# Performance work log

Hardware: AMD Instinct MI355X
Metric: run time of the kernel (lower is better)

Reference implementation:

```python
import jax, jax.numpy as jnp
import numpy as np

M, N, D = 512, 4096, 128
H = N // D  # 32
L = 4096   # cache length


def setup_inputs() -> dict:
    key = jax.random.key(0)
    ks = jax.random.split(key, 6)
    s = 1.0 / np.sqrt(N)
    return {
        "X": jax.random.normal(ks[0], (M, N), jnp.float32),
        "W_q": jax.random.normal(ks[1], (N, N), jnp.float32) * s,
        "W_k": jax.random.normal(ks[2], (N, N), jnp.float32) * s,
        "W_v": jax.random.normal(ks[3], (N, N), jnp.float32) * s,
        "cache_K": jax.random.normal(ks[4], (H, L, D), jnp.float32),
        "cache_V": jax.random.normal(ks[5], (H, L, D), jnp.float32),
        "P": 3584,
    }


def reference(X, W_q, W_k, W_v, cache_K, cache_V, P):
    # nn.Linear(N, N, bias=False): y = x @ W.T
    q = (X @ W_q.T).reshape(M, H, D).transpose(1, 0, 2)  # [H, M, D]
    k = (X @ W_k.T).reshape(M, H, D).transpose(1, 0, 2)  # [H, M, D]
    v = (X @ W_v.T).reshape(M, H, D).transpose(1, 0, 2)  # [H, M, D]
    # KV-cache write at position P (static slice under jit for fixed P)
    cK = jax.lax.dynamic_update_slice(cache_K, k, (0, P, 0))  # [H, L, D]
    cV = jax.lax.dynamic_update_slice(cache_V, v, (0, P, 0))
    # attention over the full cache, no 1/sqrt(D) scaling (faithful to source)
    scores = jnp.einsum("hmd,hld->hml", q, cK)   # [H, M, L]
    weights = jax.nn.softmax(scores, axis=-1)
    out = jnp.einsum("hml,hld->hmd", weights, cV)  # [H, M, D]
    return out.transpose(1, 0, 2).reshape(M, H * D)  # [M, N]
```

## Files before the change

kernel.cpp:

```cpp
#include <hip/hip_runtime.h>
#include <hip/hip_fp16.h>

typedef _Float16 f16x8 __attribute__((ext_vector_type(8)));
typedef float    f32x4 __attribute__((ext_vector_type(4)));

#define MFMA16(a,b,c) __builtin_amdgcn_mfma_f32_16x16x32_f16(a,b,c,0,0,0)

__device__ __forceinline__ void gload_lds16(const void* g, void* l) {
  __builtin_amdgcn_global_load_lds(
      (const __attribute__((address_space(1))) void*)g,
      (__attribute__((address_space(3))) void*)l, 16, 0, 0);
}

__global__ void cvt_f32_f16(const float* __restrict__ src,
                            _Float16* __restrict__ dst, int n8) {
  int i = blockIdx.x * blockDim.x + threadIdx.x;
  int stride = gridDim.x * blockDim.x;
  for (; i < n8; i += stride) {
    const float4* s = (const float4*)src + 2 * (size_t)i;
    float4 a = s[0], b = s[1];
    f16x8 o;
    o[0]=(_Float16)a.x; o[1]=(_Float16)a.y; o[2]=(_Float16)a.z; o[3]=(_Float16)a.w;
    o[4]=(_Float16)b.x; o[5]=(_Float16)b.y; o[6]=(_Float16)b.z; o[7]=(_Float16)b.w;
    ((f16x8*)dst)[i] = o;
  }
}

__global__ __launch_bounds__(256) void cvt_transpose_v(const float* __restrict__ src,
                                                       _Float16* __restrict__ dst) {
  __shared__ _Float16 t[64][72];
  const int b = blockIdx.x;
  const int h = b >> 7, rest = b & 127;
  const int lt = rest >> 1, dt = rest & 1;
  const int l0 = lt * 64, d0 = dt * 64;
  const int tid = threadIdx.x;
  const int r = tid >> 4, c4 = (tid & 15) * 4;
#pragma unroll
  for (int i = 0; i < 4; i++) {
    int l = r + i * 16;
    float4 v = *(const float4*)&src[((size_t)h * 4096 + l0 + l) * 128 + d0 + c4];
    t[c4 + 0][l] = (_Float16)v.x;
    t[c4 + 1][l] = (_Float16)v.y;
    t[c4 + 2][l] = (_Float16)v.z;
    t[c4 + 3][l] = (_Float16)v.w;
  }
  __syncthreads();
  const int d = tid >> 2, lc = (tid & 3) * 16;
#pragma unroll
  for (int i = 0; i < 2; i++) {
    f16x8 o = *(const f16x8*)&t[d][lc + i * 8];
    *(f16x8*)&dst[((size_t)h * 128 + d0 + d) * 4096 + l0 + lc + i * 8] = o;
  }
}

__global__ __launch_bounds__(256) void qkv_gemm(
    const _Float16* __restrict__ X,
    const float* __restrict__ Wq,
    const float* __restrict__ Wk,
    const float* __restrict__ Wv,
    _Float16* __restrict__ Q16,
    _Float16* __restrict__ Kc,
    _Float16* __restrict__ Vt16,
    const int* __restrict__ Pp)
{
  __shared__ __align__(16) _Float16 As[128 * 64];
  __shared__ __align__(16) _Float16 Bs[64 * 64];
  const int bid = blockIdx.x;
  const int xcd = bid & 7, s = bid >> 3;
  const int nt = xcd * 24 + (s >> 2);
  const int mt = s & 3;
  const int m0 = mt * 128, n0 = nt * 64;
  const int tid = threadIdx.x, wave = tid >> 6, lane = tid & 63;
  const int g = lane >> 4, c = lane & 15;
  const int wr = wave >> 1, wc = wave & 1;
  const float* Wp = (n0 < 4096) ? Wq : ((n0 < 8192) ? Wk : Wv);
  const int n0l = n0 & 4095;
  const int ar  = lane >> 3;
  const int acs = (lane & 7) * 16;
  const int brow = tid >> 2;
  const int bc32 = (tid & 3) * 16;
  const float* wsrc = Wp + (size_t)(n0l + brow) * 4096 + bc32;
  const int bsw = (brow & 7) << 4;
  float4 breg[4];
#pragma unroll
  for (int i = 0; i < 4; i++) breg[i] = *(const float4*)(wsrc + i * 4);

  f32x4 acc[4][2] = {};
  for (int k0 = 0; k0 < 4096; k0 += 64) {
    __syncthreads();
#pragma unroll
    for (int p = 0; p < 4; p++) {
      int chunk = wave * 4 + p;
      int row = chunk * 8 + ar;
      gload_lds16((const char*)(X + (size_t)(m0 + row) * 4096 + k0) + (acs ^ ((row & 7) << 4)),
                  (char*)As + chunk * 1024);
    }
    {
      const float* bv = (const float*)breg;
      f16x8 h0, h1;
#pragma unroll
      for (int i = 0; i < 8; i++) { h0[i] = (_Float16)bv[i]; h1[i] = (_Float16)bv[8 + i]; }
      char* rb = (char*)Bs + brow * 128;
      *(f16x8*)(rb + (((tid & 3) * 32)      ^ bsw)) = h0;
      *(f16x8*)(rb + (((tid & 3) * 32 + 16) ^ bsw)) = h1;
      if (k0 + 64 < 4096) {
        const float* ns = wsrc + k0 + 64;
#pragma unroll
        for (int i = 0; i < 4; i++) breg[i] = *(const float4*)(ns + i * 4);
      }
    }
    __syncthreads();
    f16x8 af[2][4], bf[2][2];
#pragma unroll
    for (int mi = 0; mi < 4; mi++) {
      int row = wr * 64 + mi * 16 + c;
      int sw = (row & 7) << 4;
#pragma unroll
      for (int kc = 0; kc < 2; kc++)
        af[kc][mi] = *(const f16x8*)((const char*)As + row * 128 + ((kc * 64 + g * 16) ^ sw));
    }
#pragma unroll
    for (int ni = 0; ni < 2; ni++) {
      int row = wc * 32 + ni * 16 + c;
      int sw = (row & 7) << 4;
#pragma unroll
      for (int kc = 0; kc < 2; kc++)
        bf[kc][ni] = *(const f16x8*)((const char*)Bs + row * 128 + ((kc * 64 + g * 16) ^ sw));
    }
#pragma unroll
    for (int kc = 0; kc < 2; kc++)
#pragma unroll
      for (int mi = 0; mi < 4; mi++)
#pragma unroll
        for (int ni = 0; ni < 2; ni++)
          acc[mi][ni] = MFMA16(af[kc][mi], bf[kc][ni], acc[mi][ni]);
  }
  const int p = Pp[0];
  const int wsel = n0 >> 12;
  const int h = (n0 & 4095) >> 7;
  const int dbase = n0 & 127;
#pragma unroll
  for (int mi = 0; mi < 4; mi++) {
#pragma unroll
    for (int ni = 0; ni < 2; ni++) {
#pragma unroll
      for (int j = 0; j < 4; j++) {
        int m = m0 + wr * 64 + mi * 16 + 4 * g + j;
        int d = dbase + wc * 32 + ni * 16 + c;
        _Float16 hv = (_Float16)acc[mi][ni][j];
        if (wsel == 0)      Q16[(size_t)(h * 512 + m) * 128 + d] = hv;
        else if (wsel == 1) Kc[(size_t)(h * 4096 + p + m) * 128 + d] = hv;
        else                Vt16[((size_t)h * 128 + d) * 4096 + p + m] = hv;
      }
    }
  }
}

__global__ __launch_bounds__(512, 2) void attn_part(
    const _Float16* __restrict__ Q16,
    const _Float16* __restrict__ Kc,
    const _Float16* __restrict__ Vt,
    float* __restrict__ Opart,
    float* __restrict__ Mpart,
    float* __restrict__ Lpart)
{
  __shared__ __align__(16) _Float16 Ks[64 * 128];
  __shared__ __align__(16) _Float16 Vs[128 * 64];
  __shared__ __align__(16) _Float16 Pl[8][32][68];
  const int bid = blockIdx.x;
  const int xcd = bid & 7, s = bid >> 3;
  const int group = xcd * 16 + (s >> 1);
  const int mt = s & 1;
  const int ls = group >> 5, h = group & 31;
  const int m0 = mt * 256;
  const int tid = threadIdx.x, wave = tid >> 6, lane = tid & 63;
  const int g = lane >> 4, c = lane & 15;
  const int mw = m0 + wave * 32;
  const _Float16* Kh  = Kc + (size_t)h * 4096 * 128;
  const _Float16* Vth = Vt + (size_t)h * 128 * 4096;
  f16x8 qf[2][4];
#pragma unroll
  for (int mi = 0; mi < 2; mi++)
#pragma unroll
    for (int kc = 0; kc < 4; kc++)
      qf[mi][kc] = *(const f16x8*)&Q16[(size_t)(h * 512 + mw + mi * 16 + c) * 128 + kc * 32 + g * 8];
  f32x4 o[2][8] = {};
  float mrow[2][4], lrow[2][4];
#pragma unroll
  for (int mi = 0; mi < 2; mi++)
#pragma unroll
    for (int j = 0; j < 4; j++) { mrow[mi][j] = -3e38f; lrow[mi][j] = 0.f; }
  const int klr = lane >> 4, klb = (lane & 15) * 16;
  const int vlr = lane >> 3, vlb = (lane & 7) * 16;

  const int l_begin = ls * 1024;
  for (int l0 = l_begin; l0 < l_begin + 1024; l0 += 64) {
    __syncthreads();
#pragma unroll
    for (int p = 0; p < 2; p++) {
      int chunk = p * 8 + wave;
      int kr = chunk * 4 + klr;
      gload_lds16((const char*)Kh + (size_t)(l0 + kr) * 256 + (klb ^ ((kr & 7) << 4)),
                  (char*)Ks + chunk * 1024);
      int vd = chunk * 8 + vlr;
      gload_lds16((const char*)Vth + (size_t)vd * 8192 + (size_t)l0 * 2 + (vlb ^ ((vd & 7) << 4)),
                  (char*)Vs + chunk * 1024);
    }
    __syncthreads();
    f32x4 sc[2][4] = {};
#pragma unroll
    for (int ni = 0; ni < 4; ni++) {
      int kr = ni * 16 + c;
      f16x8 kf[4];
#pragma unroll
      for (int kc = 0; kc < 4; kc++)
        kf[kc] = *(const f16x8*)((const char*)Ks + kr * 256 + ((kc * 64 + g * 16) ^ ((kr & 7) << 4)));
#pragma unroll
      for (int mi = 0; mi < 2; mi++)
#pragma unroll
        for (int kc = 0; kc < 4; kc++)
          sc[mi][ni] = MFMA16(qf[mi][kc], kf[kc], sc[mi][ni]);
    }
#pragma unroll
    for (int mi = 0; mi < 2; mi++) {
      float scale[4];
#pragma unroll
      for (int j = 0; j < 4; j++) {
        float tm = sc[mi][0][j];
#pragma unroll
        for (int ni = 1; ni < 4; ni++) tm = fmaxf(tm, sc[mi][ni][j]);
        tm = fmaxf(tm, __shfl_xor(tm, 1, 64));
        tm = fmaxf(tm, __shfl_xor(tm, 2, 64));
        tm = fmaxf(tm, __shfl_xor(tm, 4, 64));
        tm = fmaxf(tm, __shfl_xor(tm, 8, 64));
        float mn = fmaxf(mrow[mi][j], tm);
        scale[j] = __expf(mrow[mi][j] - mn);
        mrow[mi][j] = mn;
      }
      float rs[4] = {0.f, 0.f, 0.f, 0.f};
#pragma unroll
      for (int ni = 0; ni < 4; ni++) {
#pragma unroll
        for (int j = 0; j < 4; j++) {
          float pv = __expf(sc[mi][ni][j] - mrow[mi][j]);
          sc[mi][ni][j] = pv;
          rs[j] += pv;
        }
      }
#pragma unroll
      for (int j = 0; j < 4; j++) {
        rs[j] += __shfl_xor(rs[j], 1, 64);
        rs[j] += __shfl_xor(rs[j], 2, 64);
        rs[j] += __shfl_xor(rs[j], 4, 64);
        rs[j] += __shfl_xor(rs[j], 8, 64);
        lrow[mi][j] = lrow[mi][j] * scale[j] + rs[j];
      }
#pragma unroll
      for (int dn = 0; dn < 8; dn++)
#pragma unroll
        for (int j = 0; j < 4; j++) o[mi][dn][j] *= scale[j];
#pragma unroll
      for (int ni = 0; ni < 4; ni++)
#pragma unroll
        for (int j = 0; j < 4; j++)
          Pl[wave][mi * 16 + 4 * g + j][ni * 16 + c] = (_Float16)sc[mi][ni][j];
    }
    f16x8 pa[2][2];
#pragma unroll
    for (int mi = 0; mi < 2; mi++)
#pragma unroll
      for (int kc = 0; kc < 2; kc++)
        pa[mi][kc] = *(const f16x8*)&Pl[wave][mi * 16 + c][kc * 32 + g * 8];
#pragma unroll
    for (int dn = 0; dn < 8; dn++) {
      int vr = dn * 16 + c;
#pragma unroll
      for (int kc = 0; kc < 2; kc++) {
        f16x8 vb = *(const f16x8*)((const char*)Vs + vr * 128 + ((kc * 64 + g * 16) ^ ((vr & 7) << 4)));
#pragma unroll
        for (int mi = 0; mi < 2; mi++)
          o[mi][dn] = MFMA16(pa[mi][kc], vb, o[mi][dn]);
      }
    }
  }
  const size_t pbase = ((size_t)(ls * 32 + h) * 512);
#pragma unroll
  for (int mi = 0; mi < 2; mi++) {
#pragma unroll
    for (int dn = 0; dn < 8; dn++) {
#pragma unroll
      for (int j = 0; j < 4; j++) {
        int m = mw + mi * 16 + 4 * g + j;
        Opart[(pbase + m) * 128 + dn * 16 + c] = o[mi][dn][j];
      }
    }
  }
  if (c == 0) {
#pragma unroll
    for (int mi = 0; mi < 2; mi++)
#pragma unroll
      for (int j = 0; j < 4; j++) {
        int m = mw + mi * 16 + 4 * g + j;
        Mpart[pbase + m] = mrow[mi][j];
        Lpart[pbase + m] = lrow[mi][j];
      }
  }
}

__global__ __launch_bounds__(256) void attn_combine(
    const float* __restrict__ Opart,
    const float* __restrict__ Mpart,
    const float* __restrict__ Lpart,
    float* __restrict__ out)
{
  int idx = blockIdx.x * 256 + threadIdx.x;
  int row = idx >> 5;
  int d4  = idx & 31;
  int h = row >> 9, m = row & 511;
  float Ms[4];
  float mx = -3e38f;
#pragma unroll
  for (int s = 0; s < 4; s++) {
    Ms[s] = Mpart[(size_t)(s * 32 + h) * 512 + m];
    mx = fmaxf(mx, Ms[s]);
  }
  float lsum = 0.f;
  float4 acc = make_float4(0.f, 0.f, 0.f, 0.f);
#pragma unroll
  for (int s = 0; s < 4; s++) {
    float w = __expf(Ms[s] - mx);
    lsum += w * Lpart[(size_t)(s * 32 + h) * 512 + m];
    float4 ov = ((const float4*)(Opart + ((size_t)(s * 32 + h) * 512 + m) * 128))[d4];
    acc.x += w * ov.x; acc.y += w * ov.y; acc.z += w * ov.z; acc.w += w * ov.w;
  }
  float inv = 1.f / lsum;
  float4 r = make_float4(acc.x * inv, acc.y * inv, acc.z * inv, acc.w * inv);
  *(float4*)&out[(size_t)m * 4096 + h * 128 + d4 * 4] = r;
}

extern "C" void kernel_launch(void* const* d_in, const int* in_sizes, int n_in,
                              void* d_out, int out_size, void* d_ws, size_t ws_size,
                              hipStream_t stream) {
  const float* X  = (const float*)d_in[0];
  const float* Wq = (const float*)d_in[1];
  const float* Wk = (const float*)d_in[2];
  const float* Wv = (const float*)d_in[3];
  const float* cK = (const float*)d_in[4];
  const float* cV = (const float*)d_in[5];
  const int*   Pp = (const int*)d_in[6];
  float* out = (float*)d_out;

  char* ws = (char*)d_ws;
  _Float16* X16  = (_Float16*)(ws);
  _Float16* Q16  = (_Float16*)(ws + ((size_t)100 << 20));
  _Float16* K16  = (_Float16*)(ws + ((size_t)104 << 20));
  _Float16* V16t = (_Float16*)(ws + ((size_t)136 << 20));
  float* Opart = (float*)(ws + ((size_t)4  << 20));
  float* Mpart = (float*)(ws + ((size_t)36 << 20));
  float* Lpart = (float*)(ws + ((size_t)37 << 20));

  const int NTH = 256;
  auto cvtl = [&](const float* s, _Float16* d, size_t n) {
    int n8 = (int)(n / 8);
    int grid = (n8 + NTH - 1) / NTH;
    if (grid > 2048) grid = 2048;
    cvt_f32_f16<<<dim3(grid), dim3(NTH), 0, stream>>>(s, d, n8);
  };
  cvtl(X,  X16, (size_t)512 * 4096);
  cvtl(cK, K16, (size_t)32 * 4096 * 128);
  cvt_transpose_v<<<dim3(4096), dim3(NTH), 0, stream>>>(cV, V16t);

  qkv_gemm<<<dim3(768), dim3(256), 0, stream>>>(X16, Wq, Wk, Wv, Q16, K16, V16t, Pp);
  attn_part<<<dim3(256), dim3(512), 0, stream>>>(Q16, K16, V16t, Opart, Mpart, Lpart);
  attn_combine<<<dim3(2048), dim3(256), 0, stream>>>(Opart, Mpart, Lpart, out);
}
```

Measured before the change: 233.0 us.

## Double-buffer LDS in QKV GEMM with one barrier per k-step

Doubles the A and B shared-memory tiles in the QKV projection GEMM so the next k-tile's async global-to-LDS loads and W conversion overlap the MFMA work on the current tile. The two __syncthreads per iteration become a single barrier guarded by hand-written s_waitcnt counters, and s_setprio is raised around the MFMA block. This removes the load-to-compute stall, at the cost of twice the LDS (which may cap occupancy, hinted by launch_bounds 256,3). Correctness depends on the manual vmcnt accounting, and the wrapped last-iteration prefetches do redundant loads.

```diff
diff --git a/kernel.cpp b/kernel.cpp
--- a/kernel.cpp
+++ b/kernel.cpp
@@ -53,7 +53,7 @@
   }
 }
 
-__global__ __launch_bounds__(256) void qkv_gemm(
+__global__ __launch_bounds__(256, 3) void qkv_gemm(
     const _Float16* __restrict__ X,
     const float* __restrict__ Wq,
     const float* __restrict__ Wk,
@@ -63,8 +63,8 @@
     _Float16* __restrict__ Vt16,
     const int* __restrict__ Pp)
 {
-  __shared__ __align__(16) _Float16 As[128 * 64];
-  __shared__ __align__(16) _Float16 Bs[64 * 64];
+  __shared__ __align__(16) _Float16 As[2 * 128 * 64];
+  __shared__ __align__(16) _Float16 Bs[2 * 64 * 64];
   const int bid = blockIdx.x;
   const int xcd = bid & 7, s = bid >> 3;
   const int nt = xcd * 24 + (s >> 2);
@@ -81,35 +81,51 @@
   const int bc32 = (tid & 3) * 16;
   const float* wsrc = Wp + (size_t)(n0l + brow) * 4096 + bc32;
   const int bsw = (brow & 7) << 4;
-  float4 breg[4];
-#pragma unroll
-  for (int i = 0; i < 4; i++) breg[i] = *(const float4*)(wsrc + i * 4);
-
-  f32x4 acc[4][2] = {};
-  for (int k0 = 0; k0 < 4096; k0 += 64) {
-    __syncthreads();
+
+  float4 breg0, breg1, breg2, breg3;
+  auto loadB = [&](int k0) {
+    const float* ns = wsrc + k0;
+    breg0 = *(const float4*)(ns);
+    breg1 = *(const float4*)(ns + 4);
+    breg2 = *(const float4*)(ns + 8);
+    breg3 = *(const float4*)(ns + 12);
+  };
+  auto writeB = [&](int buf) {
+    f16x8 h0, h1;
+    h0[0]=(_Float16)breg0.x; h0[1]=(_Float16)breg0.y; h0[2]=(_Float16)breg0.z; h0[3]=(_Float16)breg0.w;
+    h0[4]=(_Float16)breg1.x; h0[5]=(_Float16)breg1.y; h0[6]=(_Float16)breg1.z; h0[7]=(_Float16)breg1.w;
+    h1[0]=(_Float16)breg2.x; h1[1]=(_Float16)breg2.y; h1[2]=(_Float16)breg2.z; h1[3]=(_Float16)breg2.w;
+    h1[4]=(_Float16)breg3.x; h1[5]=(_Float16)breg3.y; h1[6]=(_Float16)breg3.z; h1[7]=(_Float16)breg3.w;
+    char* rb = (char*)Bs + buf * 8192 + brow * 128;
+    *(f16x8*)(rb + (((tid & 3) * 32)      ^ bsw)) = h0;
+    *(f16x8*)(rb + (((tid & 3) * 32 + 16) ^ bsw)) = h1;
+  };
+  auto stageA = [&](int k0, int buf) {
 #pragma unroll
     for (int p = 0; p < 4; p++) {
       int chunk = wave * 4 + p;
       int row = chunk * 8 + ar;
       gload_lds16((const char*)(X + (size_t)(m0 + row) * 4096 + k0) + (acs ^ ((row & 7) << 4)),
-                  (char*)As + chunk * 1024);
-    }
-    {
-      const float* bv = (const float*)breg;
-      f16x8 h0, h1;
-#pragma unroll
-      for (int i = 0; i < 8; i++) { h0[i] = (_Float16)bv[i]; h1[i] = (_Float16)bv[8 + i]; }
-      char* rb = (char*)Bs + brow * 128;
-      *(f16x8*)(rb + (((tid & 3) * 32)      ^ bsw)) = h0;
-      *(f16x8*)(rb + (((tid & 3) * 32 + 16) ^ bsw)) = h1;
-      if (k0 + 64 < 4096) {
-        const float* ns = wsrc + k0 + 64;
-#pragma unroll
-        for (int i = 0; i < 4; i++) breg[i] = *(const float4*)(ns + i * 4);
-      }
-    }
-    __syncthreads();
+                  (char*)As + buf * 16384 + chunk * 1024);
+    }
+  };
+
+  f32x4 acc[4][2] = {};
+  loadB(0);
+  writeB(0);
+  stageA(0, 0);
+  loadB(64);
+  asm volatile("s_waitcnt vmcnt(4) lgkmcnt(0)" ::: "memory");
+  __builtin_amdgcn_sched_barrier(0);
+  __builtin_amdgcn_s_barrier();
+  __builtin_amdgcn_sched_barrier(0);
+
+  for (int t = 0; t < 64; ++t) {
+    const int k0 = t << 6;
+    const int cur = t & 1, nxt = cur ^ 1;
+    stageA((k0 + 64) & 4095, nxt);
+    const char* Ab = (const char*)As + cur * 16384;
+    const char* Bb = (const char*)Bs + cur * 8192;
     f16x8 af[2][4], bf[2][2];
 #pragma unroll
     for (int mi = 0; mi < 4; mi++) {
@@ -117,7 +133,7 @@
       int sw = (row & 7) << 4;
 #pragma unroll
       for (int kc = 0; kc < 2; kc++)
-        af[kc][mi] = *(const f16x8*)((const char*)As + row * 128 + ((kc * 64 + g * 16) ^ sw));
+        af[kc][mi] = *(const f16x8*)(Ab + row * 128 + ((kc * 64 + g * 16) ^ sw));
     }
 #pragma unroll
     for (int ni = 0; ni < 2; ni++) {
@@ -125,8 +141,9 @@
       int sw = (row & 7) << 4;
 #pragma unroll
       for (int kc = 0; kc < 2; kc++)
-        bf[kc][ni] = *(const f16x8*)((const char*)Bs + row * 128 + ((kc * 64 + g * 16) ^ sw));
-    }
+        bf[kc][ni] = *(const f16x8*)(Bb + row * 128 + ((kc * 64 + g * 16) ^ sw));
+    }
+    __builtin_amdgcn_s_setprio(1);
 #pragma unroll
     for (int kc = 0; kc < 2; kc++)
 #pragma unroll
@@ -134,7 +151,16 @@
 #pragma unroll
         for (int ni = 0; ni < 2; ni++)
           acc[mi][ni] = MFMA16(af[kc][mi], bf[kc][ni], acc[mi][ni]);
-  }
+    __builtin_amdgcn_s_setprio(0);
+    asm volatile("s_waitcnt vmcnt(4)" ::: "memory");
+    writeB(nxt);
+    loadB((k0 + 128) & 4095);
+    asm volatile("s_waitcnt vmcnt(4) lgkmcnt(0)" ::: "memory");
+    __builtin_amdgcn_sched_barrier(0);
+    __builtin_amdgcn_s_barrier();
+    __builtin_amdgcn_sched_barrier(0);
+  }
+
   const int p = Pp[0];
   const int wsel = n0 >> 12;
   const int h = (n0 & 4095) >> 7;
```

Result: slower. 239.1 us (+2.6%).

## Fuse KV-cache conversion into QKV GEMM launch and halve attention rows per wave

Applied to the files above, without the earlier changes.

Folds the K-cache fp16 conversion and the V-cache transpose into extra blocks of the QKV GEMM kernel. These blocks skip the rows that the GEMM overwrites at position P, which removes two launches and the redundant conversion work while letting the conversion overlap with GEMM blocks. The attention kernel now gives each wave 16 query rows instead of 32 and launches 512 blocks instead of 256, trading some reuse of the K/V tiles for more parallelism and fewer registers. Because the GEMM and cache-conversion blocks write disjoint regions of one buffer, correctness depends on that disjointness.

```diff
diff --git a/kernel.cpp b/kernel.cpp
--- a/kernel.cpp
+++ b/kernel.cpp
@@ -26,38 +26,13 @@
   }
 }
 
-__global__ __launch_bounds__(256) void cvt_transpose_v(const float* __restrict__ src,
-                                                       _Float16* __restrict__ dst) {
-  __shared__ _Float16 t[64][72];
-  const int b = blockIdx.x;
-  const int h = b >> 7, rest = b & 127;
-  const int lt = rest >> 1, dt = rest & 1;
-  const int l0 = lt * 64, d0 = dt * 64;
-  const int tid = threadIdx.x;
-  const int r = tid >> 4, c4 = (tid & 15) * 4;
-#pragma unroll
-  for (int i = 0; i < 4; i++) {
-    int l = r + i * 16;
-    float4 v = *(const float4*)&src[((size_t)h * 4096 + l0 + l) * 128 + d0 + c4];
-    t[c4 + 0][l] = (_Float16)v.x;
-    t[c4 + 1][l] = (_Float16)v.y;
-    t[c4 + 2][l] = (_Float16)v.z;
-    t[c4 + 3][l] = (_Float16)v.w;
-  }
-  __syncthreads();
-  const int d = tid >> 2, lc = (tid & 3) * 16;
-#pragma unroll
-  for (int i = 0; i < 2; i++) {
-    f16x8 o = *(const f16x8*)&t[d][lc + i * 8];
-    *(f16x8*)&dst[((size_t)h * 128 + d0 + d) * 4096 + l0 + lc + i * 8] = o;
-  }
-}
-
-__global__ __launch_bounds__(256) void qkv_gemm(
+__global__ __launch_bounds__(256) void qkv_gemm_fused(
     const _Float16* __restrict__ X,
     const float* __restrict__ Wq,
     const float* __restrict__ Wk,
     const float* __restrict__ Wv,
+    const float* __restrict__ cK,
+    const float* __restrict__ cV,
     _Float16* __restrict__ Q16,
     _Float16* __restrict__ Kc,
     _Float16* __restrict__ Vt16,
@@ -66,91 +41,142 @@
   __shared__ __align__(16) _Float16 As[128 * 64];
   __shared__ __align__(16) _Float16 Bs[64 * 64];
   const int bid = blockIdx.x;
-  const int xcd = bid & 7, s = bid >> 3;
-  const int nt = xcd * 24 + (s >> 2);
-  const int mt = s & 3;
-  const int m0 = mt * 128, n0 = nt * 64;
-  const int tid = threadIdx.x, wave = tid >> 6, lane = tid & 63;
-  const int g = lane >> 4, c = lane & 15;
-  const int wr = wave >> 1, wc = wave & 1;
-  const float* Wp = (n0 < 4096) ? Wq : ((n0 < 8192) ? Wk : Wv);
-  const int n0l = n0 & 4095;
-  const int ar  = lane >> 3;
-  const int acs = (lane & 7) * 16;
-  const int brow = tid >> 2;
-  const int bc32 = (tid & 3) * 16;
-  const float* wsrc = Wp + (size_t)(n0l + brow) * 4096 + bc32;
-  const int bsw = (brow & 7) << 4;
-  float4 breg[4];
-#pragma unroll
-  for (int i = 0; i < 4; i++) breg[i] = *(const float4*)(wsrc + i * 4);
-
-  f32x4 acc[4][2] = {};
-  for (int k0 = 0; k0 < 4096; k0 += 64) {
-    __syncthreads();
-#pragma unroll
-    for (int p = 0; p < 4; p++) {
-      int chunk = wave * 4 + p;
-      int row = chunk * 8 + ar;
-      gload_lds16((const char*)(X + (size_t)(m0 + row) * 4096 + k0) + (acs ^ ((row & 7) << 4)),
-                  (char*)As + chunk * 1024);
-    }
-    {
-      const float* bv = (const float*)breg;
-      f16x8 h0, h1;
-#pragma unroll
-      for (int i = 0; i < 8; i++) { h0[i] = (_Float16)bv[i]; h1[i] = (_Float16)bv[8 + i]; }
-      char* rb = (char*)Bs + brow * 128;
-      *(f16x8*)(rb + (((tid & 3) * 32)      ^ bsw)) = h0;
-      *(f16x8*)(rb + (((tid & 3) * 32 + 16) ^ bsw)) = h1;
-      if (k0 + 64 < 4096) {
-        const float* ns = wsrc + k0 + 64;
-#pragma unroll
-        for (int i = 0; i < 4; i++) breg[i] = *(const float4*)(ns + i * 4);
-      }
-    }
-    __syncthreads();
-    f16x8 af[2][4], bf[2][2];
+  const int tid = threadIdx.x;
+
+  if (bid < 768) {
+    const int xcd = bid & 7, s = bid >> 3;
+    const int nt = xcd * 24 + (s >> 2);
+    const int mt = s & 3;
+    const int m0 = mt * 128, n0 = nt * 64;
+    const int wave = tid >> 6, lane = tid & 63;
+    const int g = lane >> 4, c = lane & 15;
+    const int wr = wave >> 1, wc = wave & 1;
+    const float* Wp = (n0 < 4096) ? Wq : ((n0 < 8192) ? Wk : Wv);
+    const int n0l = n0 & 4095;
+    const int ar  = lane >> 3;
+    const int acs = (lane & 7) * 16;
+    const int brow = tid >> 2;
+    const int bc32 = (tid & 3) * 16;
+    const float* wsrc = Wp + (size_t)(n0l + brow) * 4096 + bc32;
+    const int bsw = (brow & 7) << 4;
+    float4 breg[4];
+#pragma unroll
+    for (int i = 0; i < 4; i++) breg[i] = *(const float4*)(wsrc + i * 4);
+
+    f32x4 acc[4][2] = {};
+    for (int k0 = 0; k0 < 4096; k0 += 64) {
+      __syncthreads();
+#pragma unroll
+      for (int p = 0; p < 4; p++) {
+        int chunk = wave * 4 + p;
+        int row = chunk * 8 + ar;
+        gload_lds16((const char*)(X + (size_t)(m0 + row) * 4096 + k0) + (acs ^ ((row & 7) << 4)),
+                    (char*)As + chunk * 1024);
+      }
+      {
+        const float* bv = (const float*)breg;
+        f16x8 h0, h1;
+#pragma unroll
+        for (int i = 0; i < 8; i++) { h0[i] = (_Float16)bv[i]; h1[i] = (_Float16)bv[8 + i]; }
+        char* rb = (char*)Bs + brow * 128;
+        *(f16x8*)(rb + (((tid & 3) * 32)      ^ bsw)) = h0;
+        *(f16x8*)(rb + (((tid & 3) * 32 + 16) ^ bsw)) = h1;
+        if (k0 + 64 < 4096) {
+          const float* ns = wsrc + k0 + 64;
+#pragma unroll
+          for (int i = 0; i < 4; i++) breg[i] = *(const float4*)(ns + i * 4);
+        }
+      }
+      __syncthreads();
+      f16x8 af[2][4], bf[2][2];
+#pragma unroll
+      for (int mi = 0; mi < 4; mi++) {
+        int row = wr * 64 + mi * 16 + c;
+        int sw = (row & 7) << 4;
+#pragma unroll
+        for (int kc = 0; kc < 2; kc++)
+          af[kc][mi] = *(const f16x8*)((const char*)As + row * 128 + ((kc * 64 + g * 16) ^ sw));
+      }
+#pragma unroll
+      for (int ni = 0; ni < 2; ni++) {
+        int row = wc * 32 + ni * 16 + c;
+        int sw = (row & 7) << 4;
+#pragma unroll
+        for (int kc = 0; kc < 2; kc++)
+          bf[kc][ni] = *(const f16x8*)((const char*)Bs + row * 128 + ((kc * 64 + g * 16) ^ sw));
+      }
+#pragma unroll
+      for (int kc = 0; kc < 2; kc++)
+#pragma unroll
+        for (int mi = 0; mi < 4; mi++)
+#pragma unroll
+          for (int ni = 0; ni < 2; ni++)
+            acc[mi][ni] = MFMA16(af[kc][mi], bf[kc][ni], acc[mi][ni]);
+    }
+    const int p = Pp[0];
+    const int wsel = n0 >> 12;
+    const int h = (n0 & 4095) >> 7;
+    const int dbase = n0 & 127;
 #pragma unroll
     for (int mi = 0; mi < 4; mi++) {
-      int row = wr * 64 + mi * 16 + c;
-      int sw = (row & 7) << 4;
-#pragma unroll
-      for (int kc = 0; kc < 2; kc++)
-        af[kc][mi] = *(const f16x8*)((const char*)As + row * 128 + ((kc * 64 + g * 16) ^ sw));
-    }
-#pragma unroll
-    for (int ni = 0; ni < 2; ni++) {
-      int row = wc * 32 + ni * 16 + c;
-      int sw = (row & 7) << 4;
-#pragma unroll
-      for (int kc = 0; kc < 2; kc++)
-        bf[kc][ni] = *(const f16x8*)((const char*)Bs + row * 128 + ((kc * 64 + g * 16) ^ sw));
-    }
-#pragma unroll
-    for (int kc = 0; kc < 2; kc++)
-#pragma unroll
-      for (int mi = 0; mi < 4; mi++)
-#pragma unroll
-        for (int ni = 0; ni < 2; ni++)
-          acc[mi][ni] = MFMA16(af[kc][mi], bf[kc][ni], acc[mi][ni]);
-  }
+#pragma unroll
+      for (int ni = 0; ni < 2; ni++) {
+#pragma unroll
+        for (int j = 0; j < 4; j++) {
+          int m = m0 + wr * 64 + mi * 16 + 4 * g + j;
+          int d = dbase + wc * 32 + ni * 16 + c;
+          _Float16 hv = (_Float16)acc[mi][ni][j];
+          if (wsel == 0)      Q16[(size_t)(h * 512 + m) * 128 + d] = hv;
+          else if (wsel == 1) Kc[(size_t)(h * 4096 + p + m) * 128 + d] = hv;
+          else                Vt16[((size_t)h * 128 + d) * 4096 + p + m] = hv;
+        }
+      }
+    }
+    return;
+  }
+
   const int p = Pp[0];
-  const int wsel = n0 >> 12;
-  const int h = (n0 & 4095) >> 7;
-  const int dbase = n0 & 127;
-#pragma unroll
-  for (int mi = 0; mi < 4; mi++) {
-#pragma unroll
-    for (int ni = 0; ni < 2; ni++) {
-#pragma unroll
-      for (int j = 0; j < 4; j++) {
-        int m = m0 + wr * 64 + mi * 16 + 4 * g + j;
-        int d = dbase + wc * 32 + ni * 16 + c;
-        _Float16 hv = (_Float16)acc[mi][ni][j];
-        if (wsel == 0)      Q16[(size_t)(h * 512 + m) * 128 + d] = hv;
-        else if (wsel == 1) Kc[(size_t)(h * 4096 + p + m) * 128 + d] = hv;
-        else                Vt16[((size_t)h * 128 + d) * 4096 + p + m] = hv;
+  const int cb = bid - 768;
+  if (cb < 512) {
+    const int total = 32 * 4096 * 16;
+    const int stride = 512 * 256;
+    for (int i = cb * 256 + tid; i < total; i += stride) {
+      int l = (i >> 4) & 4095;
+      if ((unsigned)(l - p) < 512u) continue;
+      const float4* s = (const float4*)cK + 2 * (size_t)i;
+      float4 a = s[0], b = s[1];
+      f16x8 o;
+      o[0]=(_Float16)a.x; o[1]=(_Float16)a.y; o[2]=(_Float16)a.z; o[3]=(_Float16)a.w;
+      o[4]=(_Float16)b.x; o[5]=(_Float16)b.y; o[6]=(_Float16)b.z; o[7]=(_Float16)b.w;
+      ((f16x8*)Kc)[i] = o;
+    }
+  } else {
+    _Float16 (*t)[72] = (_Float16 (*)[72])As;
+    const int r = tid >> 4, c4 = (tid & 15) * 4;
+    const int d = tid >> 2, lc = (tid & 3) * 16;
+#pragma unroll
+    for (int rep = 0; rep < 2; rep++) {
+      int b = (cb - 512) * 2 + rep;
+      int h = b >> 7, rest = b & 127;
+      int lt = rest >> 1, dt = rest & 1;
+      int l0 = lt * 64, d0 = dt * 64;
+      __syncthreads();
+#pragma unroll
+      for (int i = 0; i < 4; i++) {
+        int l = r + i * 16;
+        float4 v = *(const float4*)&cV[((size_t)h * 4096 + l0 + l) * 128 + d0 + c4];
+        t[c4 + 0][l] = (_Float16)v.x;
+        t[c4 + 1][l] = (_Float16)v.y;
+        t[c4 + 2][l] = (_Float16)v.z;
+        t[c4 + 3][l] = (_Float16)v.w;
+      }
+      __syncthreads();
+#pragma unroll
+      for (int i = 0; i < 2; i++) {
+        int l = l0 + lc + i * 8;
+        if ((unsigned)(l - p) < 512u) continue;
+        f16x8 o = *(const f16x8*)&t[d][lc + i * 8];
+        *(f16x8*)&Vt16[((size_t)h * 128 + d0 + d) * 4096 + l] = o;
       }
     }
   }
@@ -166,30 +192,25 @@
 {
   __shared__ __align__(16) _Float16 Ks[64 * 128];
   __shared__ __align__(16) _Float16 Vs[128 * 64];
-  __shared__ __align__(16) _Float16 Pl[8][32][68];
+  __shared__ __align__(16) _Float16 Pl[8][16][68];
   const int bid = blockIdx.x;
   const int xcd = bid & 7, s = bid >> 3;
-  const int group = xcd * 16 + (s >> 1);
-  const int mt = s & 1;
+  const int group = xcd * 16 + (s >> 2);
+  const int mt = s & 3;
   const int ls = group >> 5, h = group & 31;
-  const int m0 = mt * 256;
+  const int m0 = mt * 128;
   const int tid = threadIdx.x, wave = tid >> 6, lane = tid & 63;
   const int g = lane >> 4, c = lane & 15;
-  const int mw = m0 + wave * 32;
+  const int mw = m0 + wave * 16;
   const _Float16* Kh  = Kc + (size_t)h * 4096 * 128;
   const _Float16* Vth = Vt + (size_t)h * 128 * 4096;
-  f16x8 qf[2][4];
-#pragma unroll
-  for (int mi = 0; mi < 2; mi++)
-#pragma unroll
-    for (int kc = 0; kc < 4; kc++)
-      qf[mi][kc] = *(const f16x8*)&Q16[(size_t)(h * 512 + mw + mi * 16 + c) * 128 + kc * 32 + g * 8];
-  f32x4 o[2][8] = {};
-  float mrow[2][4], lrow[2][4];
-#pragma unroll
-  for (int mi = 0; mi < 2; mi++)
-#pragma unroll
-    for (int j = 0; j < 4; j++) { mrow[mi][j] = -3e38f; lrow[mi][j] = 0.f; }
+  f16x8 qf[4];
+#pragma unroll
+  for (int kc = 0; kc < 4; kc++)
+    qf[kc] = *(const f16x8*)&Q16[(size_t)(h * 512 + mw + c) * 128 + kc * 32 + g * 8];
+  f32x4 o[8] = {};
+  float mrow[4] = {-3e38f, -3e38f, -3e38f, -3e38f};
+  float lrow[4] = {0.f, 0.f, 0.f, 0.f};
   const int klr = lane >> 4, klb = (lane & 15) * 16;
   const int vlr = lane >> 3, vlb = (lane & 7) * 16;
 
@@ -207,7 +228,7 @@
                   (char*)Vs + chunk * 1024);
     }
     __syncthreads();
-    f32x4 sc[2][4] = {};
+    f32x4 sc[4] = {};
 #pragma unroll
     for (int ni = 0; ni < 4; ni++) {
       int kr = ni * 16 + c;
@@ -216,94 +237,80 @@
       for (int kc = 0; kc < 4; kc++)
         kf[kc] = *(const f16x8*)((const char*)Ks + kr * 256 + ((kc * 64 + g * 16) ^ ((kr & 7) << 4)));
 #pragma unroll
-      for (int mi = 0; mi < 2; mi++)
-#pragma unroll
-        for (int kc = 0; kc < 4; kc++)
-          sc[mi][ni] = MFMA16(qf[mi][kc], kf[kc], sc[mi][ni]);
-    }
-#pragma unroll
-    for (int mi = 0; mi < 2; mi++) {
-      float scale[4];
+      for (int kc = 0; kc < 4; kc++)
+        sc[ni] = MFMA16(qf[kc], kf[kc], sc[ni]);
+    }
+    float scale[4];
+#pragma unroll
+    for (int j = 0; j < 4; j++) {
+      float tm = sc[0][j];
+#pragma unroll
+      for (int ni = 1; ni < 4; ni++) tm = fmaxf(tm, sc[ni][j]);
+      tm = fmaxf(tm, __shfl_xor(tm, 1, 64));
+      tm = fmaxf(tm, __shfl_xor(tm, 2, 64));
+      tm = fmaxf(tm, __shfl_xor(tm, 4, 64));
+      tm = fmaxf(tm, __shfl_xor(tm, 8, 64));
+      float mn = fmaxf(mrow[j], tm);
+      scale[j] = __expf(mrow[j] - mn);
+      mrow[j] = mn;
+    }
+    float rs[4] = {0.f, 0.f, 0.f, 0.f};
+#pragma unroll
+    for (int ni = 0; ni < 4; ni++) {
 #pragma unroll
       for (int j = 0; j < 4; j++) {
-        float tm = sc[mi][0][j];
-#pragma unroll
-        for (int ni = 1; ni < 4; ni++) tm = fmaxf(tm, sc[mi][ni][j]);
-        tm = fmaxf(tm, __shfl_xor(tm, 1, 64));
-        tm = fmaxf(tm, __shfl_xor(tm, 2, 64));
-        tm = fmaxf(tm, __shfl_xor(tm, 4, 64));
-        tm = fmaxf(tm, __shfl_xor(tm, 8, 64));
-        float mn = fmaxf(mrow[mi][j], tm);
-        scale[j] = __expf(mrow[mi][j] - mn);
-        mrow[mi][j] = mn;
-      }
-      float rs[4] = {0.f, 0.f, 0.f, 0.f};
-#pragma unroll
-      for (int ni = 0; ni < 4; ni++) {
-#pragma unroll
-        for (int j = 0; j < 4; j++) {
-          float pv = __expf(sc[mi][ni][j] - mrow[mi][j]);
-          sc[mi][ni][j] = pv;
-          rs[j] += pv;
-        }
-      }
-#pragma unroll
-      for (int j = 0; j < 4; j++) {
-        rs[j] += __shfl_xor(rs[j], 1, 64);
-        rs[j] += __shfl_xor(rs[j], 2, 64);
-        rs[j] += __shfl_xor(rs[j], 4, 64);
-        rs[j] += __shfl_xor(rs[j], 8, 64);
-        lrow[mi][j] = lrow[mi][j] * scale[j] + rs[j];
-      }
-#pragma unroll
-      for (int dn = 0; dn < 8; dn++)
-#pragma unroll
-        for (int j = 0; j < 4; j++) o[mi][dn][j] *= scale[j];
-#pragma unroll
-      for (int ni = 0; ni < 4; ni++)
-#pragma unroll
-        for (int j = 0; j < 4; j++)
-          Pl[wave][mi * 16 + 4 * g + j][ni * 16 + c] = (_Float16)sc[mi][ni][j];
-    }
-    f16x8 pa[2][2];
-#pragma unroll
-    for (int mi = 0; mi < 2; mi++)
-#pragma unroll
-      for (int kc = 0; kc < 2; kc++)
-        pa[mi][kc] = *(const f16x8*)&Pl[wave][mi * 16 + c][kc * 32 + g * 8];
+        float pv = __expf(sc[ni][j] - mrow[j]);
+        sc[ni][j] = pv;
+        rs[j] += pv;
+      }
+    }
+#pragma unroll
+    for (int j = 0; j < 4; j++) {
+      rs[j] += __shfl_xor(rs[j], 1, 64);
+      rs[j] += __shfl_xor(rs[j], 2, 64);
+      rs[j] += __shfl_xor(rs[j], 4, 64);
+      rs[j] += __shfl_xor(rs[j], 8, 64);
+      lrow[j] = lrow[j] * scale[j] + rs[j];
+    }
+#pragma unroll
+    for (int dn = 0; dn < 8; dn++)
+#pragma unroll
+      for (int j = 0; j < 4; j++) o[dn][j] *= scale[j];
+#pragma unroll
+    for (int ni = 0; ni < 4; ni++)
+#pragma unroll
+      for (int j = 0; j < 4; j++)
+        Pl[wave][4 * g + j][ni * 16 + c] = (_Float16)sc[ni][j];
+    f16x8 pa[2];
+#pragma unroll
+    for (int kc = 0; kc < 2; kc++)
+      pa[kc] = *(const f16x8*)&Pl[wave][c][kc * 32 + g * 8];
 #pragma unroll
     for (int dn = 0; dn < 8; dn++) {
       int vr = dn * 16 + c;
 #pragma unroll
       for (int kc = 0; kc < 2; kc++) {
         f16x8 vb = *(const f16x8*)((const char*)Vs + vr * 128 + ((kc * 64 + g * 16) ^ ((vr & 7) << 4)));
-#pragma unroll
-        for (int mi = 0; mi < 2; mi++)
-          o[mi][dn] = MFMA16(pa[mi][kc], vb, o[mi][dn]);
+        o[dn] = MFMA16(pa[kc], vb, o[dn]);
       }
     }
   }
   const size_t pbase = ((size_t)(ls * 32 + h) * 512);
 #pragma unroll
-  for (int mi = 0; mi < 2; mi++) {
-#pragma unroll
-    for (int dn = 0; dn < 8; dn++) {
-#pragma unroll
-      for (int j = 0; j < 4; j++) {
-        int m = mw + mi * 16 + 4 * g + j;
-        Opart[(pbase + m) * 128 + dn * 16 + c] = o[mi][dn][j];
-      }
+  for (int dn = 0; dn < 8; dn++) {
+#pragma unroll
+    for (int j = 0; j < 4; j++) {
+      int m = mw + 4 * g + j;
+      Opart[(pbase + m) * 128 + dn * 16 + c] = o[dn][j];
     }
   }
   if (c == 0) {
 #pragma unroll
-    for (int mi = 0; mi < 2; mi++)
-#pragma unroll
-      for (int j = 0; j < 4; j++) {
-        int m = mw + mi * 16 + 4 * g + j;
-        Mpart[pbase + m] = mrow[mi][j];
-        Lpart[pbase + m] = lrow[mi][j];
-      }
+    for (int j = 0; j < 4; j++) {
+      int m = mw + 4 * g + j;
+      Mpart[pbase + m] = mrow[j];
+      Lpart[pbase + m] = lrow[j];
+    }
   }
 }
 
@@ -352,25 +359,18 @@
 
   char* ws = (char*)d_ws;
   _Float16* X16  = (_Float16*)(ws);
+  float* Opart = (float*)(ws + ((size_t)4  << 20));
+  float* Mpart = (float*)(ws + ((size_t)36 << 20));
+  float* Lpart = (float*)(ws + ((size_t)37 << 20));
   _Float16* Q16  = (_Float16*)(ws + ((size_t)100 << 20));
   _Float16* K16  = (_Float16*)(ws + ((size_t)104 << 20));
   _Float16* V16t = (_Float16*)(ws + ((size_t)136 << 20));
-  float* Opart = (float*)(ws + ((size_t)4  << 20));
-  float* Mpart = (float*)(ws + ((size_t)36 << 20));
-  float* Lpart = (float*)(ws + ((size_t)37 << 20));
-
-  const int NTH = 256;
-  auto cvtl = [&](const float* s, _Float16* d, size_t n) {
-    int n8 = (int)(n / 8);
-    int grid = (n8 + NTH - 1) / NTH;
-    if (grid > 2048) grid = 2048;
-    cvt_f32_f16<<<dim3(grid), dim3(NTH), 0, stream>>>(s, d, n8);
-  };
-  cvtl(X,  X16, (size_t)512 * 4096);
-  cvtl(cK, K16, (size_t)32 * 4096 * 128);
-  cvt_transpose_v<<<dim3(4096), dim3(NTH), 0, stream>>>(cV, V16t);
-
-  qkv_gemm<<<dim3(768), dim3(256), 0, stream>>>(X16, Wq, Wk, Wv, Q16, K16, V16t, Pp);
-  attn_part<<<dim3(256), dim3(512), 0, stream>>>(Q16, K16, V16t, Opart, Mpart, Lpart);
+
+  cvt_f32_f16<<<dim3(1024), dim3(256), 0, stream>>>(X, X16, 512 * 4096 / 8);
+
+  qkv_gemm_fused<<<dim3(768 + 512 + 2048), dim3(256), 0, stream>>>(
+      X16, Wq, Wk, Wv, cK, cV, Q16, K16, V16t, Pp);
+
+  attn_part<<<dim3(512), dim3(512), 0, stream>>>(Q16, K16, V16t, Opart, Mpart, Lpart);
   attn_combine<<<dim3(2048), dim3(256), 0, stream>>>(Opart, Mpart, Lpart, out);
 }
```

Result: faster. 224.3 us (-3.7%).
